# Performance work log

Hardware: AMD Instinct MI355X
Metric: run time of the kernel (lower is better)

## Reference

```python
import jax, jax.numpy as jnp
import numpy as np

N, E, D, R = 50000, 800000, 256, 16


def setup_inputs() -> dict:
    key = jax.random.key(0)
    ks = jax.random.split(key, 6)
    x = jax.random.normal(ks[0], (N, D), dtype=jnp.float32)
    edge_index = jax.random.randint(ks[1], (2, E), 0, N)
    edge_type = jax.random.randint(ks[2], (E,), 0, R)
    # FastRGCNConv params (num_bases=None): full relation weight, root weight, bias
    weight = jax.random.normal(ks[3], (R, D, 1), dtype=jnp.float32) / np.float32(np.sqrt(D))
    root = jax.random.normal(ks[4], (D, 1), dtype=jnp.float32) / np.float32(np.sqrt(D))
    bias = jnp.zeros((1,), dtype=jnp.float32)
    return dict(x=x, edge_index=edge_index, edge_type=edge_type,
                weight=weight, root=root, bias=bias)


def reference(x, edge_index, edge_type, weight, root, bias):
    n = x.shape[0]
    src, dst = edge_index[0], edge_index[1]  # messages flow src (j) -> dst (i)
    # per-edge relation-wise transform: (x_j @ W[r])  with out_channels == 1
    w_e = weight[edge_type, :, 0]                   # [E, D] gather of relation weights
    msg = jnp.sum(x[src] * w_e, axis=-1)            # [E] per-edge scalar message
    # mean aggregation over incoming edges (scatter-add / degree)
    agg = jax.ops.segment_sum(msg, dst, num_segments=n)                   # [N]
    cnt = jax.ops.segment_sum(jnp.ones_like(msg), dst, num_segments=n)    # [N]
    mean = agg / jnp.maximum(cnt, 1.0)
    # root transform + bias, then tanh nonlinearity (min_score is None)
    score = jnp.tanh(mean + (x @ root)[:, 0] + bias[0])                   # [N]
    x_out = x * score[:, None]
    return x_out, score
```

## Files before the change

### kernel.cpp

```cpp
#include <hip/hip_runtime.h>
#include <math.h>

#define D 256
#define NREL 16
#define CHUNK 6250
#define BPC 32

__global__ __launch_bounds__(256) void rgcn_y_kernel(
    const float* __restrict__ x, const float* __restrict__ w,
    const float* __restrict__ root, float* __restrict__ y,
    float* __restrict__ xr, int n)
{
    __shared__ float lds[64 * 65];
    const int t = threadIdx.x;
    const int nl = t & 63;
    const int rg = __builtin_amdgcn_readfirstlane(t >> 6);
    const int node = blockIdx.x * 64 + nl;
    const int base = blockIdx.x * 64;

    const float* w0 = w + (size_t)(rg * 4 + 0) * D;
    const float* w1 = w + (size_t)(rg * 4 + 1) * D;
    const float* w2 = w + (size_t)(rg * 4 + 2) * D;
    const float* w3 = w + (size_t)(rg * 4 + 3) * D;
    const float* w4 = (rg == 3) ? root : w0;

    float acc0 = 0.f, acc1 = 0.f, acc2 = 0.f, acc3 = 0.f, accR = 0.f;

    for (int c = 0; c < 4; ++c) {
        #pragma unroll
        for (int j = 0; j < 4; ++j) {
            int flat = j * 256 + t;
            int snl  = flat >> 4;
            int f4   = flat & 15;
            int gn   = base + snl;
            float4 v = make_float4(0.f, 0.f, 0.f, 0.f);
            if (gn < n)
                v = *reinterpret_cast<const float4*>(
                        x + (size_t)gn * D + c * 64 + f4 * 4);
            int a = snl * 65 + f4 * 4;
            lds[a + 0] = v.x; lds[a + 1] = v.y;
            lds[a + 2] = v.z; lds[a + 3] = v.w;
        }
        __syncthreads();

        const float* wc0 = w0 + c * 64;
        const float* wc1 = w1 + c * 64;
        const float* wc2 = w2 + c * 64;
        const float* wc3 = w3 + c * 64;
        const float* wc4 = w4 + c * 64;
        #pragma unroll
        for (int d = 0; d < 64; ++d) {
            float xv = lds[nl * 65 + d];
            acc0 = fmaf(xv, wc0[d], acc0);
            acc1 = fmaf(xv, wc1[d], acc1);
            acc2 = fmaf(xv, wc2[d], acc2);
            acc3 = fmaf(xv, wc3[d], acc3);
            accR = fmaf(xv, wc4[d], accR);
        }
        __syncthreads();
    }

    if (node < n) {
        float4 o; o.x = acc0; o.y = acc1; o.z = acc2; o.w = acc3;
        *reinterpret_cast<float4*>(y + (size_t)node * NREL + rg * 4) = o;
        if (rg == 3) xr[node] = accR;
    }
}

__global__ __launch_bounds__(1024) void rgcn_edge_scan_kernel(
    const int* __restrict__ src, const int* __restrict__ dst,
    const int* __restrict__ et, const float* __restrict__ y,
    float2* __restrict__ partial, int e, int sl)
{
    __shared__ float lsum[CHUNK];
    __shared__ float lcnt[CHUNK];
    const int t = threadIdx.x;
    const int c = blockIdx.x / BPC;
    const int b = blockIdx.x % BPC;
    const int base = c * CHUNK;

    for (int j = t; j < CHUNK; j += 1024) { lsum[j] = 0.f; lcnt[j] = 0.f; }
    __syncthreads();

    const int slice0 = b * sl;
    const int rem = e - slice0;
    if (rem > 0) {
        const int gmax = (min(sl, rem) + 3) >> 2;
        for (int g = t; g < gmax; g += 1024) {
            int idx = slice0 + g * 4;
            if (idx + 3 < e) {
                int4 d4 = *reinterpret_cast<const int4*>(dst + idx);
                int4 s4 = *reinterpret_cast<const int4*>(src + idx);
                int4 r4 = *reinterpret_cast<const int4*>(et + idx);
                int loc0 = d4.x - base, loc1 = d4.y - base;
                int loc2 = d4.z - base, loc3 = d4.w - base;
                if ((unsigned)loc0 < (unsigned)CHUNK) {
                    atomicAdd(&lsum[loc0], y[(size_t)s4.x * NREL + r4.x]);
                    atomicAdd(&lcnt[loc0], 1.0f);
                }
                if ((unsigned)loc1 < (unsigned)CHUNK) {
                    atomicAdd(&lsum[loc1], y[(size_t)s4.y * NREL + r4.y]);
                    atomicAdd(&lcnt[loc1], 1.0f);
                }
                if ((unsigned)loc2 < (unsigned)CHUNK) {
                    atomicAdd(&lsum[loc2], y[(size_t)s4.z * NREL + r4.z]);
                    atomicAdd(&lcnt[loc2], 1.0f);
                }
                if ((unsigned)loc3 < (unsigned)CHUNK) {
                    atomicAdd(&lsum[loc3], y[(size_t)s4.w * NREL + r4.w]);
                    atomicAdd(&lcnt[loc3], 1.0f);
                }
            } else {
                for (int k = idx; k < e; ++k) {
                    int loc = dst[k] - base;
                    if ((unsigned)loc < (unsigned)CHUNK) {
                        atomicAdd(&lsum[loc], y[(size_t)src[k] * NREL + et[k]]);
                        atomicAdd(&lcnt[loc], 1.0f);
                    }
                }
            }
        }
    }
    __syncthreads();

    float2* p = partial + ((size_t)(c * BPC + b)) * CHUNK;
    for (int j = t; j < CHUNK; j += 1024)
        p[j] = make_float2(lsum[j], lcnt[j]);
}

__global__ __launch_bounds__(256) void rgcn_finish_kernel(
    const float2* __restrict__ partial, const float* __restrict__ xr,
    const float* __restrict__ bias, const float* __restrict__ x,
    float* __restrict__ out_x, float* __restrict__ out_score, int n)
{
    __shared__ float sc[64];
    const int t = threadIdx.x;
    const int base = blockIdx.x * 64;

    if (t < 64) {
        int node = base + t;
        if (node < n) {
            int c = node / CHUNK;
            int j = node - c * CHUNK;
            const float2* p = partial + (size_t)c * BPC * CHUNK + j;
            float s = 0.f, cN = 0.f;
            #pragma unroll 8
            for (int b = 0; b < BPC; ++b) {
                float2 v = p[(size_t)b * CHUNK];
                s += v.x; cN += v.y;
            }
            float m = s / fmaxf(cN, 1.0f);
            float v = tanhf(m + xr[node] + bias[0]);
            sc[t] = v;
            out_score[node] = v;
        }
    }
    __syncthreads();

    #pragma unroll 4
    for (int k = 0; k < 16; ++k) {
        int flat = k * 256 + t;
        int nl = flat >> 6;
        int f4 = flat & 63;
        int node = base + nl;
        if (node < n) {
            float s = sc[nl];
            float4 v = *reinterpret_cast<const float4*>(
                           x + (size_t)node * D + f4 * 4);
            v.x *= s; v.y *= s; v.z *= s; v.w *= s;
            *reinterpret_cast<float4*>(out_x + (size_t)node * D + f4 * 4) = v;
        }
    }
}

__global__ __launch_bounds__(256) void rgcn_reduce_score_kernel(
    const float2* __restrict__ partial, const float* __restrict__ xr,
    const float* __restrict__ bias, float* __restrict__ score, int n)
{
    int i = blockIdx.x * 256 + threadIdx.x;
    if (i < n) {
        int c = i / CHUNK;
        int j = i - c * CHUNK;
        const float2* p = partial + (size_t)c * BPC * CHUNK + j;
        float s = 0.f, cN = 0.f;
        #pragma unroll 8
        for (int b = 0; b < BPC; ++b) {
            float2 v = p[(size_t)b * CHUNK];
            s += v.x; cN += v.y;
        }
        float m = s / fmaxf(cN, 1.0f);
        score[i] = tanhf(m + xr[i] + bias[0]);
    }
}

__global__ __launch_bounds__(256) void rgcn_scale_kernel(
    const float* __restrict__ x, const float* __restrict__ score,
    float* __restrict__ xo, int n)
{
    int gid = blockIdx.x * 256 + threadIdx.x;
    int node = gid >> 6;
    int f4 = gid & 63;
    if (node < n) {
        float s = score[node];
        float4 v = *reinterpret_cast<const float4*>(
                       x + (size_t)node * D + f4 * 4);
        v.x *= s; v.y *= s; v.z *= s; v.w *= s;
        *reinterpret_cast<float4*>(xo + (size_t)node * D + f4 * 4) = v;
    }
}

extern "C" void kernel_launch(void* const* d_in, const int* in_sizes, int n_in,
                              void* d_out, int out_size, void* d_ws, size_t ws_size,
                              hipStream_t stream)
{
    const float* x    = (const float*)d_in[0];
    const int*   ei   = (const int*)d_in[1];
    const int*   et   = (const int*)d_in[2];
    const float* w    = (const float*)d_in[3];
    const float* root = (const float*)d_in[4];
    const float* bias = (const float*)d_in[5];

    const int n = in_sizes[0] / D;
    const int e = in_sizes[2];

    float* out       = (float*)d_out;
    float* out_x     = out;
    float* out_score = out + (size_t)n * D;

    const int C = (n + CHUNK - 1) / CHUNK;
    const int sl = ((((e + BPC - 1) / BPC) + 3) & ~3);

    const size_t part_f = (size_t)C * BPC * CHUNK * 2;
    const size_t need_f = part_f + (size_t)n * (NREL + 1);
    const bool use_ws = (ws_size >= need_f * sizeof(float));

    float* sb;
    if (use_ws)
        sb = (float*)d_ws;
    else {
        size_t ts = (((size_t)n * D - need_f) & ~(size_t)1);
        sb = out_x + ts;
    }
    float2* partial = (float2*)sb;
    float*  y  = sb + part_f;
    float*  xr = y + (size_t)n * NREL;

    dim3 blk(256);
    rgcn_y_kernel<<<dim3((n + 63) / 64), blk, 0, stream>>>(x, w, root, y, xr, n);

    rgcn_edge_scan_kernel<<<dim3(C * BPC), dim3(1024), 0, stream>>>(
        ei, ei + e, et, y, partial, e, sl);

    if (use_ws) {
        rgcn_finish_kernel<<<dim3((n + 63) / 64), blk, 0, stream>>>(
            partial, xr, bias, x, out_x, out_score, n);
    } else {
        rgcn_reduce_score_kernel<<<dim3((n + 255) / 256), blk, 0, stream>>>(
            partial, xr, bias, out_score, n);
        rgcn_scale_kernel<<<dim3((int)(((size_t)n * 64 + 255) / 256)), blk, 0, stream>>>(
            x, out_score, out_x, n);
    }
}
```

Baseline: 63.40 us.

## Double-buffer x tiles in y kernel and parallelize partial reduction in finish

```diff
diff --git a/kernel.cpp b/kernel.cpp
--- a/kernel.cpp
+++ b/kernel.cpp
@@ -6,12 +6,14 @@
 #define CHUNK 6250
 #define BPC 32
 
+typedef float f4v __attribute__((ext_vector_type(4)));
+
 __global__ __launch_bounds__(256) void rgcn_y_kernel(
     const float* __restrict__ x, const float* __restrict__ w,
     const float* __restrict__ root, float* __restrict__ y,
     float* __restrict__ xr, int n)
 {
-    __shared__ float lds[64 * 65];
+    __shared__ float lds[2][64 * 65];
     const int t = threadIdx.x;
     const int nl = t & 63;
     const int rg = __builtin_amdgcn_readfirstlane(t >> 6);
@@ -26,22 +28,43 @@
 
     float acc0 = 0.f, acc1 = 0.f, acc2 = 0.f, acc3 = 0.f, accR = 0.f;
 
+    int snlj[4], f4j[4];
+    #pragma unroll
+    for (int j = 0; j < 4; ++j) {
+        int flat = j * 256 + t;
+        snlj[j] = flat >> 4;
+        f4j[j]  = flat & 15;
+    }
+
+    float4 vv[4];
+    #pragma unroll
+    for (int j = 0; j < 4; ++j) {
+        int gn = base + snlj[j];
+        vv[j] = make_float4(0.f, 0.f, 0.f, 0.f);
+        if (gn < n)
+            vv[j] = *reinterpret_cast<const float4*>(
+                        x + (size_t)gn * D + f4j[j] * 4);
+    }
+    #pragma unroll
+    for (int j = 0; j < 4; ++j) {
+        int a = snlj[j] * 65 + f4j[j] * 4;
+        lds[0][a + 0] = vv[j].x; lds[0][a + 1] = vv[j].y;
+        lds[0][a + 2] = vv[j].z; lds[0][a + 3] = vv[j].w;
+    }
+    __syncthreads();
+
+    #pragma unroll
     for (int c = 0; c < 4; ++c) {
-        #pragma unroll
-        for (int j = 0; j < 4; ++j) {
-            int flat = j * 256 + t;
-            int snl  = flat >> 4;
-            int f4   = flat & 15;
-            int gn   = base + snl;
-            float4 v = make_float4(0.f, 0.f, 0.f, 0.f);
-            if (gn < n)
-                v = *reinterpret_cast<const float4*>(
-                        x + (size_t)gn * D + c * 64 + f4 * 4);
-            int a = snl * 65 + f4 * 4;
-            lds[a + 0] = v.x; lds[a + 1] = v.y;
-            lds[a + 2] = v.z; lds[a + 3] = v.w;
-        }
-        __syncthreads();
+        if (c < 3) {
+            #pragma unroll
+            for (int j = 0; j < 4; ++j) {
+                int gn = base + snlj[j];
+                vv[j] = make_float4(0.f, 0.f, 0.f, 0.f);
+                if (gn < n)
+                    vv[j] = *reinterpret_cast<const float4*>(
+                                x + (size_t)gn * D + (c + 1) * 64 + f4j[j] * 4);
+            }
+        }
 
         const float* wc0 = w0 + c * 64;
         const float* wc1 = w1 + c * 64;
@@ -50,14 +73,26 @@
         const float* wc4 = w4 + c * 64;
         #pragma unroll
         for (int d = 0; d < 64; ++d) {
-            float xv = lds[nl * 65 + d];
+            float xv = lds[c & 1][nl * 65 + d];
             acc0 = fmaf(xv, wc0[d], acc0);
             acc1 = fmaf(xv, wc1[d], acc1);
             acc2 = fmaf(xv, wc2[d], acc2);
             acc3 = fmaf(xv, wc3[d], acc3);
             accR = fmaf(xv, wc4[d], accR);
         }
-        __syncthreads();
+
+        if (c < 3) {
+            __syncthreads();
+            #pragma unroll
+            for (int j = 0; j < 4; ++j) {
+                int a = snlj[j] * 65 + f4j[j] * 4;
+                lds[(c + 1) & 1][a + 0] = vv[j].x;
+                lds[(c + 1) & 1][a + 1] = vv[j].y;
+                lds[(c + 1) & 1][a + 2] = vv[j].z;
+                lds[(c + 1) & 1][a + 3] = vv[j].w;
+            }
+            __syncthreads();
+        }
     }
 
     if (node < n) {
@@ -133,23 +168,37 @@
     const float* __restrict__ bias, const float* __restrict__ x,
     float* __restrict__ out_x, float* __restrict__ out_score, int n)
 {
-    __shared__ float sc[64];
+    __shared__ float ssum[32], scnt[32], sc[32];
     const int t = threadIdx.x;
-    const int base = blockIdx.x * 64;
-
-    if (t < 64) {
-        int node = base + t;
+    const int base = blockIdx.x * 32;
+
+    if (t < 32) { ssum[t] = 0.f; scnt[t] = 0.f; }
+    __syncthreads();
+
+    {
+        int nl = t & 31;
+        int bg = t >> 5;
+        int node = base + nl;
+        float s = 0.f, cN = 0.f;
         if (node < n) {
             int c = node / CHUNK;
             int j = node - c * CHUNK;
             const float2* p = partial + (size_t)c * BPC * CHUNK + j;
-            float s = 0.f, cN = 0.f;
-            #pragma unroll 8
-            for (int b = 0; b < BPC; ++b) {
-                float2 v = p[(size_t)b * CHUNK];
+            #pragma unroll
+            for (int b = 0; b < 4; ++b) {
+                float2 v = p[(size_t)(bg * 4 + b) * CHUNK];
                 s += v.x; cN += v.y;
             }
-            float m = s / fmaxf(cN, 1.0f);
+        }
+        atomicAdd(&ssum[nl], s);
+        atomicAdd(&scnt[nl], cN);
+    }
+    __syncthreads();
+
+    if (t < 32) {
+        int node = base + t;
+        if (node < n) {
+            float m = ssum[t] / fmaxf(scnt[t], 1.0f);
             float v = tanhf(m + xr[node] + bias[0]);
             sc[t] = v;
             out_score[node] = v;
@@ -157,18 +206,19 @@
     }
     __syncthreads();
 
-    #pragma unroll 4
-    for (int k = 0; k < 16; ++k) {
-        int flat = k * 256 + t;
-        int nl = flat >> 6;
-        int f4 = flat & 63;
+    #pragma unroll
+    for (int k = 0; k < 8; ++k) {
+        int nl = k * 4 + (t >> 6);
+        int f4 = t & 63;
         int node = base + nl;
         if (node < n) {
             float s = sc[nl];
             float4 v = *reinterpret_cast<const float4*>(
                            x + (size_t)node * D + f4 * 4);
             v.x *= s; v.y *= s; v.z *= s; v.w *= s;
-            *reinterpret_cast<float4*>(out_x + (size_t)node * D + f4 * 4) = v;
+            f4v vo = {v.x, v.y, v.z, v.w};
+            __builtin_nontemporal_store(
+                vo, (f4v*)(out_x + (size_t)node * D + f4 * 4));
         }
     }
 }
@@ -252,7 +302,7 @@
         ei, ei + e, et, y, partial, e, sl);
 
     if (use_ws) {
-        rgcn_finish_kernel<<<dim3((n + 63) / 64), blk, 0, stream>>>(
+        rgcn_finish_kernel<<<dim3((n + 31) / 32), blk, 0, stream>>>(
             partial, xr, bias, x, out_x, out_score, n);
     } else {
         rgcn_reduce_score_kernel<<<dim3((n + 255) / 256), blk, 0, stream>>>(
```

After: 105.6 us. 1.67x slower.

## Halve y-kernel staging passes and parallelize finish-kernel partial reduction

Applied to the files above, without the earlier changes.

```diff
diff --git a/kernel.cpp b/kernel.cpp
--- a/kernel.cpp
+++ b/kernel.cpp
@@ -5,13 +5,16 @@
 #define NREL 16
 #define CHUNK 6250
 #define BPC 32
+#define LDST 129
+
+typedef float f4v __attribute__((ext_vector_type(4)));
 
 __global__ __launch_bounds__(256) void rgcn_y_kernel(
     const float* __restrict__ x, const float* __restrict__ w,
     const float* __restrict__ root, float* __restrict__ y,
     float* __restrict__ xr, int n)
 {
-    __shared__ float lds[64 * 65];
+    __shared__ float lds[64 * LDST];
     const int t = threadIdx.x;
     const int nl = t & 63;
     const int rg = __builtin_amdgcn_readfirstlane(t >> 6);
@@ -26,38 +29,39 @@
 
     float acc0 = 0.f, acc1 = 0.f, acc2 = 0.f, acc3 = 0.f, accR = 0.f;
 
-    for (int c = 0; c < 4; ++c) {
+    #pragma unroll
+    for (int h = 0; h < 2; ++h) {
         #pragma unroll
-        for (int j = 0; j < 4; ++j) {
-            int flat = j * 256 + t;
-            int snl  = flat >> 4;
-            int f4   = flat & 15;
+        for (int k = 0; k < 8; ++k) {
+            int flat = k * 256 + t;
+            int snl  = flat >> 5;
+            int f4i  = flat & 31;
             int gn   = base + snl;
             float4 v = make_float4(0.f, 0.f, 0.f, 0.f);
             if (gn < n)
                 v = *reinterpret_cast<const float4*>(
-                        x + (size_t)gn * D + c * 64 + f4 * 4);
-            int a = snl * 65 + f4 * 4;
+                        x + (size_t)gn * D + h * 128 + f4i * 4);
+            int a = snl * LDST + f4i * 4;
             lds[a + 0] = v.x; lds[a + 1] = v.y;
             lds[a + 2] = v.z; lds[a + 3] = v.w;
         }
         __syncthreads();
 
-        const float* wc0 = w0 + c * 64;
-        const float* wc1 = w1 + c * 64;
-        const float* wc2 = w2 + c * 64;
-        const float* wc3 = w3 + c * 64;
-        const float* wc4 = w4 + c * 64;
-        #pragma unroll
-        for (int d = 0; d < 64; ++d) {
-            float xv = lds[nl * 65 + d];
-            acc0 = fmaf(xv, wc0[d], acc0);
-            acc1 = fmaf(xv, wc1[d], acc1);
-            acc2 = fmaf(xv, wc2[d], acc2);
-            acc3 = fmaf(xv, wc3[d], acc3);
-            accR = fmaf(xv, wc4[d], accR);
-        }
-        __syncthreads();
+        const float* h0 = w0 + h * 128;
+        const float* h1 = w1 + h * 128;
+        const float* h2 = w2 + h * 128;
+        const float* h3 = w3 + h * 128;
+        const float* h4 = w4 + h * 128;
+        #pragma unroll 16
+        for (int d = 0; d < 128; ++d) {
+            float xv = lds[nl * LDST + d];
+            acc0 = fmaf(xv, h0[d], acc0);
+            acc1 = fmaf(xv, h1[d], acc1);
+            acc2 = fmaf(xv, h2[d], acc2);
+            acc3 = fmaf(xv, h3[d], acc3);
+            accR = fmaf(xv, h4[d], accR);
+        }
+        if (h == 0) __syncthreads();
     }
 
     if (node < n) {
@@ -133,23 +137,37 @@
     const float* __restrict__ bias, const float* __restrict__ x,
     float* __restrict__ out_x, float* __restrict__ out_score, int n)
 {
-    __shared__ float sc[64];
+    __shared__ float ssum[32], scnt[32], sc[32];
     const int t = threadIdx.x;
-    const int base = blockIdx.x * 64;
-
-    if (t < 64) {
-        int node = base + t;
+    const int base = blockIdx.x * 32;
+
+    if (t < 32) { ssum[t] = 0.f; scnt[t] = 0.f; }
+    __syncthreads();
+
+    {
+        int nl = t & 31;
+        int bg = t >> 5;
+        int node = base + nl;
+        float s = 0.f, cN = 0.f;
         if (node < n) {
             int c = node / CHUNK;
             int j = node - c * CHUNK;
             const float2* p = partial + (size_t)c * BPC * CHUNK + j;
-            float s = 0.f, cN = 0.f;
-            #pragma unroll 8
-            for (int b = 0; b < BPC; ++b) {
-                float2 v = p[(size_t)b * CHUNK];
+            #pragma unroll
+            for (int b = 0; b < 4; ++b) {
+                float2 v = p[(size_t)(bg * 4 + b) * CHUNK];
                 s += v.x; cN += v.y;
             }
-            float m = s / fmaxf(cN, 1.0f);
+        }
+        atomicAdd(&ssum[nl], s);
+        atomicAdd(&scnt[nl], cN);
+    }
+    __syncthreads();
+
+    if (t < 32) {
+        int node = base + t;
+        if (node < n) {
+            float m = ssum[t] / fmaxf(scnt[t], 1.0f);
             float v = tanhf(m + xr[node] + bias[0]);
             sc[t] = v;
             out_score[node] = v;
@@ -157,18 +175,19 @@
     }
     __syncthreads();
 
-    #pragma unroll 4
-    for (int k = 0; k < 16; ++k) {
-        int flat = k * 256 + t;
-        int nl = flat >> 6;
-        int f4 = flat & 63;
+    #pragma unroll
+    for (int k = 0; k < 8; ++k) {
+        int nl = k * 4 + (t >> 6);
+        int f4 = t & 63;
         int node = base + nl;
         if (node < n) {
             float s = sc[nl];
             float4 v = *reinterpret_cast<const float4*>(
                            x + (size_t)node * D + f4 * 4);
             v.x *= s; v.y *= s; v.z *= s; v.w *= s;
-            *reinterpret_cast<float4*>(out_x + (size_t)node * D + f4 * 4) = v;
+            f4v vo = {v.x, v.y, v.z, v.w};
+            __builtin_nontemporal_store(
+                vo, (f4v*)(out_x + (size_t)node * D + f4 * 4));
         }
     }
 }
@@ -252,7 +271,7 @@
         ei, ei + e, et, y, partial, e, sl);
 
     if (use_ws) {
-        rgcn_finish_kernel<<<dim3((n + 63) / 64), blk, 0, stream>>>(
+        rgcn_finish_kernel<<<dim3((n + 31) / 32), blk, 0, stream>>>(
             partial, xr, bias, x, out_x, out_score, n);
     } else {
         rgcn_reduce_score_kernel<<<dim3((n + 255) / 256), blk, 0, stream>>>(
```

Measured after the change: 61.22 us. 1.04x faster.
